# Kernel tuning notes

Hardware: AMD Instinct MI355X
Metric: run time of the kernel (lower is better)

## Reference

```python
import jax, jax.numpy as jnp
import numpy as np

B = 1_000_000   # batched RHS evaluation points
T = 1461        # days of forcing data (~4 years)
H = 16          # hidden width of ET_net / Q_net


def _step(x):
    # step_fct from models.common_net: smooth Heaviside
    return (jnp.tanh(5.0 * x) + 1.0) * 0.5


def _mlp(x, w1, b1, w2, b2, w3, b3):
    h = jnp.tanh(x @ w1 + b1)
    h = jnp.tanh(h @ w2 + b2)
    return (h @ w3 + b3)[:, 0]


def setup_inputs() -> dict:
    key = jax.random.key(0)
    ks = jax.random.split(key, 12)
    inp = {}
    inp["t"] = jax.random.uniform(ks[0], (B,), jnp.float32) * (T - 1)
    # S[:,0]=S_snow, S[:,1]=S_water  (storages in mm)
    inp["S"] = jax.random.uniform(ks[1], (B, 2), jnp.float32) * 500.0
    inp["ts"] = jnp.arange(T, dtype=jnp.float32)
    inp["precp_series"] = jax.random.uniform(ks[2], (T,), jnp.float32) * 20.0
    inp["temp_series"] = jax.random.uniform(ks[3], (T,), jnp.float32) * 30.0 - 10.0
    inp["lday_series"] = jax.random.uniform(ks[4], (T,), jnp.float32) * 0.2 + 0.3

    def lin(k, i, o):
        return jax.random.normal(k, (i, o), jnp.float32) * (1.0 / np.sqrt(i))

    inp["et_w1"] = lin(ks[5], 3, H); inp["et_b1"] = jnp.zeros((H,), jnp.float32)
    inp["et_w2"] = lin(ks[6], H, H); inp["et_b2"] = jnp.zeros((H,), jnp.float32)
    inp["et_w3"] = lin(ks[7], H, 1); inp["et_b3"] = jnp.zeros((1,), jnp.float32)
    inp["q_w1"] = lin(ks[8], 2, H); inp["q_b1"] = jnp.zeros((H,), jnp.float32)
    inp["q_w2"] = lin(ks[9], H, H); inp["q_b2"] = jnp.zeros((H,), jnp.float32)
    inp["q_w3"] = lin(ks[10], H, 1); inp["q_b3"] = jnp.zeros((1,), jnp.float32)
    # physics params: f, Smax, Qmax, Df, Tmax, Tmin
    inp["f"] = jnp.float32(0.5)
    inp["Smax"] = jnp.float32(1000.0)
    inp["Qmax"] = jnp.float32(20.0)
    inp["Df"] = jnp.float32(2.0)
    inp["Tmax"] = jnp.float32(1.0)
    inp["Tmin"] = jnp.float32(-1.0)
    return inp


def reference(t, S, ts, precp_series, temp_series, lday_series,
              et_w1, et_b1, et_w2, et_b2, et_w3, et_b3,
              q_w1, q_b1, q_w2, q_b2, q_w3, q_b3,
              f, Smax, Qmax, Df, Tmax, Tmin):
    # clamp_parameters()
    f = jnp.clip(f, 0.0, 1.0)
    Smax = jnp.clip(Smax, 100.0, 1500.0)
    Qmax = jnp.clip(Qmax, 10.0, 50.0)
    Df = jnp.clip(Df, 0.01, 5.0)
    Tmax = jnp.clip(Tmax, 0.0, 3.0)
    Tmin = jnp.clip(Tmin, -3.0, 0.0)

    # forcing interpolation (interp.evaluate(t))
    precp = jnp.interp(t, ts, precp_series)
    temp = jnp.interp(t, ts, temp_series)
    lday = jnp.interp(t, ts, lday_series)

    S_snow, S_water = S[:, 0], S[:, 1]

    ET = _mlp(jnp.stack([S_snow, S_water, temp], axis=-1),
              et_w1, et_b1, et_w2, et_b2, et_w3, et_b3)  # [B]
    Q = _mlp(jnp.stack([S_water, precp], axis=-1),
             q_w1, q_b1, q_w2, q_b2, q_w3, q_b3)          # [B]

    # M: snowmelt
    melt = _step(temp - Tmax) * _step(S_snow) * jnp.minimum(S_snow, Df * (temp - Tmax))
    # Ps / Pr: snow / rain partition of precipitation
    dS_1 = _step(Tmin - temp) * precp - melt
    dS_2 = (_step(temp - Tmin) * precp + melt
            - _step(S_water) * lday * jnp.exp(ET)
            - _step(S_water) * jnp.exp(Q))
    return jnp.stack([dS_1, dS_2], axis=-1)  # [B, 2]
```

## Files before the change

### kernel.cpp

```cpp
#include <hip/hip_runtime.h>

#define TLEN 1461
#define L2E      1.44269504088896340736f
#define TWO_L2E  2.88539008177792681472f

typedef __bf16 bf16x8 __attribute__((ext_vector_type(8)));
typedef float f32x16 __attribute__((ext_vector_type(16)));

union FragU { unsigned u[4]; bf16x8 f; };

__device__ __forceinline__ float tanh_pre(float y) {
    float e = __builtin_amdgcn_exp2f(y);
    return fmaf(-2.0f, __builtin_amdgcn_rcpf(e + 1.0f), 1.0f);
}
__device__ __forceinline__ float step_fn(float x) {
    float e = __builtin_amdgcn_exp2f(x * -14.4269504088896341f);
    return __builtin_amdgcn_rcpf(1.0f + e);
}
__device__ __forceinline__ unsigned cvt_pk_bf16(float lo, float hi) {
    unsigned r;
    asm("v_cvt_pk_bf16_f32 %0, %1, %2" : "=v"(r) : "v"(lo), "v"(hi));
    return r;
}
__device__ __forceinline__ void plswap(unsigned &a, unsigned &b) {
    asm("v_permlane32_swap_b32 %0, %1" : "+v"(a), "+v"(b));
}
__device__ __forceinline__ float plswap_add(float a, float b) {
    unsigned ua = __float_as_uint(a), ub = __float_as_uint(b);
    plswap(ua, ub);
    return __uint_as_float(ua) + __uint_as_float(ub);
}

__device__ __forceinline__ void pack_b(const float h[16], FragU &ba, FragU &bb) {
    unsigned lo0 = cvt_pk_bf16(h[0], h[1]),   lo1 = cvt_pk_bf16(h[2], h[3]);
    unsigned lo2 = cvt_pk_bf16(h[4], h[5]),   lo3 = cvt_pk_bf16(h[6], h[7]);
    unsigned hi0 = cvt_pk_bf16(h[8], h[9]),   hi1 = cvt_pk_bf16(h[10], h[11]);
    unsigned hi2 = cvt_pk_bf16(h[12], h[13]), hi3 = cvt_pk_bf16(h[14], h[15]);
    plswap(lo0, hi0); plswap(lo1, hi1); plswap(lo2, hi2); plswap(lo3, hi3);
    ba.u[0] = lo0; ba.u[1] = lo1; ba.u[2] = lo2; ba.u[3] = lo3;
    bb.u[0] = hi0; bb.u[1] = hi1; bb.u[2] = hi2; bb.u[3] = hi3;
}

__device__ __forceinline__ float tail(const FragU a2, const float jb[8],
                                      const float w3v[8], float b3half,
                                      const FragU ba, const FragU bb) {
    f32x16 c0, c1;
#pragma unroll
    for (int r = 0; r < 8; ++r) { c0[r] = jb[r]; c1[r] = jb[r]; }
    c0 = __builtin_amdgcn_mfma_f32_32x32x16_bf16(a2.f, ba.f, c0, 0, 0, 0);
    c1 = __builtin_amdgcn_mfma_f32_32x32x16_bf16(a2.f, bb.f, c1, 0, 0, 0);

    float p0 = b3half, p1 = b3half;
#pragma unroll
    for (int r = 0; r < 8; ++r) {
        p0 = fmaf(tanh_pre(c0[r]), w3v[r], p0);
        p1 = fmaf(tanh_pre(c1[r]), w3v[r], p1);
    }
    return plswap_add(p0, p1);
}

__global__ __launch_bounds__(256) void hydro_kernel(
    const float* __restrict__ g_t,
    const float* __restrict__ g_S,
    const float* __restrict__ g_precp,
    const float* __restrict__ g_temp,
    const float* __restrict__ g_lday,
    const float* __restrict__ g_ew1, const float* __restrict__ g_eb1,
    const float* __restrict__ g_ew2, const float* __restrict__ g_eb2,
    const float* __restrict__ g_ew3, const float* __restrict__ g_eb3,
    const float* __restrict__ g_qw1, const float* __restrict__ g_qb1,
    const float* __restrict__ g_qw2, const float* __restrict__ g_qb2,
    const float* __restrict__ g_qw3, const float* __restrict__ g_qb3,
    const float* __restrict__ g_Df, const float* __restrict__ g_Tmax,
    const float* __restrict__ g_Tmin,
    float* __restrict__ g_out, int B)
{
    __shared__ __align__(16) float4 s_tbl[TLEN];

    const int tx = threadIdx.x;
    for (int i = tx; i < TLEN; i += 256) {
        s_tbl[i] = make_float4(g_precp[i], g_temp[i], g_lday[i], 0.0f);
    }
    __syncthreads();

    const int lane = tx & 63;
    const int m  = lane & 31;
    const int kg = lane >> 5;

    FragU a2e, a2q;
#pragma unroll
    for (int p = 0; p < 4; ++p) {
        const int k0 = 8 * kg + 2 * p, k1 = k0 + 1;
        const int mm = (m < 16) ? m : 0;
        const float s = (m < 16) ? TWO_L2E : 0.0f;
        a2e.u[p] = cvt_pk_bf16(s * g_ew2[k0 * 16 + mm], s * g_ew2[k1 * 16 + mm]);
        a2q.u[p] = cvt_pk_bf16(s * g_qw2[k0 * 16 + mm], s * g_qw2[k1 * 16 + mm]);
    }
    float jbe[8], jbq[8], w3ve[8], w3vq[8];
#pragma unroll
    for (int r = 0; r < 8; ++r) {
        const int j = (r & 3) + 8 * (r >> 2) + 4 * kg;
        jbe[r]  = TWO_L2E * g_eb2[j];
        jbq[r]  = TWO_L2E * g_qb2[j];
        w3ve[r] = L2E * g_ew3[j];
        w3vq[r] = L2E * g_qw3[j];
    }
    const float b3e_half = (kg == 0) ? L2E * g_eb3[0] : 0.0f;
    const float b3q_half = (kg == 0) ? L2E * g_qb3[0] : 0.0f;

    const float Df   = fminf(fmaxf(g_Df[0],   0.01f), 5.0f);
    const float Tmax = fminf(fmaxf(g_Tmax[0], 0.0f),  3.0f);
    const float Tmin = fminf(fmaxf(g_Tmin[0], -3.0f), 0.0f);

    const int i = blockIdx.x * 256 + tx;
    const int ic = (i < B) ? i : (B - 1);

    const float tv = g_t[ic];
    const float2 Sv = reinterpret_cast<const float2*>(g_S)[ic];
    const float S_snow = Sv.x, S_water = Sv.y;

    int idx = (int)tv;
    idx = max(0, min(idx, TLEN - 2));
    const float fr = tv - (float)idx;
    const float4 t0 = s_tbl[idx];
    const float4 t1 = s_tbl[idx + 1];
    const float precp = fmaf(fr, t1.x - t0.x, t0.x);
    const float temp  = fmaf(fr, t1.y - t0.y, t0.y);
    const float lday  = fmaf(fr, t1.z - t0.z, t0.z);

    float h1e[16], h1q[16];
#pragma unroll
    for (int j4 = 0; j4 < 4; ++j4) {
        float4 b4 = *reinterpret_cast<const float4*>(&g_eb1[j4 * 4]);
        float4 w0 = *reinterpret_cast<const float4*>(&g_ew1[0 * 16 + j4 * 4]);
        float4 w1 = *reinterpret_cast<const float4*>(&g_ew1[1 * 16 + j4 * 4]);
        float4 w2 = *reinterpret_cast<const float4*>(&g_ew1[2 * 16 + j4 * 4]);
        h1e[j4 * 4 + 0] = tanh_pre(TWO_L2E * fmaf(temp, w2.x, fmaf(S_water, w1.x, fmaf(S_snow, w0.x, b4.x))));
        h1e[j4 * 4 + 1] = tanh_pre(TWO_L2E * fmaf(temp, w2.y, fmaf(S_water, w1.y, fmaf(S_snow, w0.y, b4.y))));
        h1e[j4 * 4 + 2] = tanh_pre(TWO_L2E * fmaf(temp, w2.z, fmaf(S_water, w1.z, fmaf(S_snow, w0.z, b4.z))));
        h1e[j4 * 4 + 3] = tanh_pre(TWO_L2E * fmaf(temp, w2.w, fmaf(S_water, w1.w, fmaf(S_snow, w0.w, b4.w))));
    }
#pragma unroll
    for (int j4 = 0; j4 < 4; ++j4) {
        float4 b4 = *reinterpret_cast<const float4*>(&g_qb1[j4 * 4]);
        float4 w0 = *reinterpret_cast<const float4*>(&g_qw1[0 * 16 + j4 * 4]);
        float4 w1 = *reinterpret_cast<const float4*>(&g_qw1[1 * 16 + j4 * 4]);
        h1q[j4 * 4 + 0] = tanh_pre(TWO_L2E * fmaf(precp, w1.x, fmaf(S_water, w0.x, b4.x)));
        h1q[j4 * 4 + 1] = tanh_pre(TWO_L2E * fmaf(precp, w1.y, fmaf(S_water, w0.y, b4.y)));
        h1q[j4 * 4 + 2] = tanh_pre(TWO_L2E * fmaf(precp, w1.z, fmaf(S_water, w0.z, b4.z)));
        h1q[j4 * 4 + 3] = tanh_pre(TWO_L2E * fmaf(precp, w1.w, fmaf(S_water, w0.w, b4.w)));
    }

    FragU bae, bbe, baq, bbq;
    pack_b(h1e, bae, bbe);
    pack_b(h1q, baq, bbq);

    const float ETs = tail(a2e, jbe, w3ve, b3e_half, bae, bbe);
    const float Qs  = tail(a2q, jbq, w3vq, b3q_half, baq, bbq);

    const float sw_step = step_fn(S_water);
    const float melt = step_fn(temp - Tmax) * step_fn(S_snow)
                     * fminf(S_snow, Df * (temp - Tmax));
    const float dS1 = step_fn(Tmin - temp) * precp - melt;
    const float dS2 = step_fn(temp - Tmin) * precp + melt
                    - sw_step * lday * __builtin_amdgcn_exp2f(ETs)
                    - sw_step * __builtin_amdgcn_exp2f(Qs);

    if (i < B) {
        reinterpret_cast<float2*>(g_out)[i] = make_float2(dS1, dS2);
    }
}

extern "C" void kernel_launch(void* const* d_in, const int* in_sizes, int n_in,
                              void* d_out, int out_size, void* d_ws, size_t ws_size,
                              hipStream_t stream)
{
    const int B = in_sizes[0];
    const int block = 256;
    const int grid = (B + block - 1) / block;
    hipLaunchKernelGGL(hydro_kernel, dim3(grid), dim3(block), 0, stream,
        (const float*)d_in[0],
        (const float*)d_in[1],
        (const float*)d_in[3],
        (const float*)d_in[4],
        (const float*)d_in[5],
        (const float*)d_in[6],  (const float*)d_in[7],
        (const float*)d_in[8],  (const float*)d_in[9],
        (const float*)d_in[10], (const float*)d_in[11],
        (const float*)d_in[12], (const float*)d_in[13],
        (const float*)d_in[14], (const float*)d_in[15],
        (const float*)d_in[16], (const float*)d_in[17],
        (const float*)d_in[21],
        (const float*)d_in[22],
        (const float*)d_in[23],
        (float*)d_out, B);
}
```

Baseline: 28.78 us.

## Process two samples per thread and fold tanh affine terms into weights

Each thread now handles two batch points, so the per-block setup (shared forcing table fill, weight fragment construction) is amortised over 512 samples and the grid is halved. The layer-3 tanh is rewritten as a sigmoid form, with its -2 scale and +1 offset folded into the output weights and bias, which removes an FMA per hidden unit. Layer-1 tanh values are packed to bf16 as soon as they are computed, and the snow/rain split reuses one step evaluation as 1-sp. Two independent sample pipelines per thread raise register pressure and may lower occupancy, and the block count falls to roughly 2k.

```diff
diff --git a/kernel.cpp b/kernel.cpp
--- a/kernel.cpp
+++ b/kernel.cpp
@@ -9,10 +9,6 @@
 
 union FragU { unsigned u[4]; bf16x8 f; };
 
-__device__ __forceinline__ float tanh_pre(float y) {
-    float e = __builtin_amdgcn_exp2f(y);
-    return fmaf(-2.0f, __builtin_amdgcn_rcpf(e + 1.0f), 1.0f);
-}
 __device__ __forceinline__ float step_fn(float x) {
     float e = __builtin_amdgcn_exp2f(x * -14.4269504088896341f);
     return __builtin_amdgcn_rcpf(1.0f + e);
@@ -31,18 +27,20 @@
     return __uint_as_float(ua) + __uint_as_float(ub);
 }
 
-__device__ __forceinline__ void pack_b(const float h[16], FragU &ba, FragU &bb) {
-    unsigned lo0 = cvt_pk_bf16(h[0], h[1]),   lo1 = cvt_pk_bf16(h[2], h[3]);
-    unsigned lo2 = cvt_pk_bf16(h[4], h[5]),   lo3 = cvt_pk_bf16(h[6], h[7]);
-    unsigned hi0 = cvt_pk_bf16(h[8], h[9]),   hi1 = cvt_pk_bf16(h[10], h[11]);
-    unsigned hi2 = cvt_pk_bf16(h[12], h[13]), hi3 = cvt_pk_bf16(h[14], h[15]);
-    plswap(lo0, hi0); plswap(lo1, hi1); plswap(lo2, hi2); plswap(lo3, hi3);
-    ba.u[0] = lo0; ba.u[1] = lo1; ba.u[2] = lo2; ba.u[3] = lo3;
-    bb.u[0] = hi0; bb.u[1] = hi1; bb.u[2] = hi2; bb.u[3] = hi3;
+__device__ __forceinline__ void quad_tanh_pack(float y0, float y1, float y2, float y3,
+                                               unsigned &wlo, unsigned &whi) {
+    float s0 = __builtin_amdgcn_rcpf(1.0f + __builtin_amdgcn_exp2f(y0));
+    float s1 = __builtin_amdgcn_rcpf(1.0f + __builtin_amdgcn_exp2f(y1));
+    float s2 = __builtin_amdgcn_rcpf(1.0f + __builtin_amdgcn_exp2f(y2));
+    float s3 = __builtin_amdgcn_rcpf(1.0f + __builtin_amdgcn_exp2f(y3));
+    float h0 = fmaf(-2.0f, s0, 1.0f), h1 = fmaf(-2.0f, s1, 1.0f);
+    float h2 = fmaf(-2.0f, s2, 1.0f), h3 = fmaf(-2.0f, s3, 1.0f);
+    wlo = cvt_pk_bf16(h0, h1);
+    whi = cvt_pk_bf16(h2, h3);
 }
 
 __device__ __forceinline__ float tail(const FragU a2, const float jb[8],
-                                      const float w3v[8], float b3half,
+                                      const float w3n[8], float pinit,
                                       const FragU ba, const FragU bb) {
     f32x16 c0, c1;
 #pragma unroll
@@ -50,13 +48,93 @@
     c0 = __builtin_amdgcn_mfma_f32_32x32x16_bf16(a2.f, ba.f, c0, 0, 0, 0);
     c1 = __builtin_amdgcn_mfma_f32_32x32x16_bf16(a2.f, bb.f, c1, 0, 0, 0);
 
-    float p0 = b3half, p1 = b3half;
+    float p0 = pinit, p1 = pinit;
 #pragma unroll
     for (int r = 0; r < 8; ++r) {
-        p0 = fmaf(tanh_pre(c0[r]), w3v[r], p0);
-        p1 = fmaf(tanh_pre(c1[r]), w3v[r], p1);
+        float s0 = __builtin_amdgcn_rcpf(1.0f + __builtin_amdgcn_exp2f(c0[r]));
+        float s1 = __builtin_amdgcn_rcpf(1.0f + __builtin_amdgcn_exp2f(c1[r]));
+        p0 = fmaf(w3n[r], s0, p0);
+        p1 = fmaf(w3n[r], s1, p1);
     }
     return plswap_add(p0, p1);
+}
+
+struct Weights {
+    FragU a2e, a2q;
+    float jbe[8], jbq[8], w3ne[8], w3nq[8];
+    float pinit_e, pinit_q;
+    float Df, Tmax, Tmin;
+};
+
+__device__ __forceinline__ float2 sample_pipeline(
+    float tv, float S_snow, float S_water,
+    const float4* __restrict__ s_tbl, const Weights &W,
+    const float* __restrict__ g_ew1, const float* __restrict__ g_eb1,
+    const float* __restrict__ g_qw1, const float* __restrict__ g_qb1)
+{
+    int idx = (int)tv;
+    idx = max(0, min(idx, TLEN - 2));
+    const float fr = tv - (float)idx;
+    const float4 t0 = s_tbl[idx];
+    const float4 t1 = s_tbl[idx + 1];
+    const float precp = fmaf(fr, t1.x - t0.x, t0.x);
+    const float temp  = fmaf(fr, t1.y - t0.y, t0.y);
+    const float lday  = fmaf(fr, t1.z - t0.z, t0.z);
+
+    unsigned elo[4], ehi[4], qlo[4], qhi[4];
+#pragma unroll
+    for (int j4 = 0; j4 < 4; ++j4) {
+        float4 b4 = *reinterpret_cast<const float4*>(&g_eb1[j4 * 4]);
+        float4 w0 = *reinterpret_cast<const float4*>(&g_ew1[0 * 16 + j4 * 4]);
+        float4 w1 = *reinterpret_cast<const float4*>(&g_ew1[1 * 16 + j4 * 4]);
+        float4 w2 = *reinterpret_cast<const float4*>(&g_ew1[2 * 16 + j4 * 4]);
+        float y0 = TWO_L2E * fmaf(temp, w2.x, fmaf(S_water, w1.x, fmaf(S_snow, w0.x, b4.x)));
+        float y1 = TWO_L2E * fmaf(temp, w2.y, fmaf(S_water, w1.y, fmaf(S_snow, w0.y, b4.y)));
+        float y2 = TWO_L2E * fmaf(temp, w2.z, fmaf(S_water, w1.z, fmaf(S_snow, w0.z, b4.z)));
+        float y3 = TWO_L2E * fmaf(temp, w2.w, fmaf(S_water, w1.w, fmaf(S_snow, w0.w, b4.w)));
+        unsigned wl, wh;
+        quad_tanh_pack(y0, y1, y2, y3, wl, wh);
+        if (j4 < 2) { elo[j4 * 2] = wl; elo[j4 * 2 + 1] = wh; }
+        else        { ehi[(j4 - 2) * 2] = wl; ehi[(j4 - 2) * 2 + 1] = wh; }
+    }
+#pragma unroll
+    for (int j4 = 0; j4 < 4; ++j4) {
+        float4 b4 = *reinterpret_cast<const float4*>(&g_qb1[j4 * 4]);
+        float4 w0 = *reinterpret_cast<const float4*>(&g_qw1[0 * 16 + j4 * 4]);
+        float4 w1 = *reinterpret_cast<const float4*>(&g_qw1[1 * 16 + j4 * 4]);
+        float y0 = TWO_L2E * fmaf(precp, w1.x, fmaf(S_water, w0.x, b4.x));
+        float y1 = TWO_L2E * fmaf(precp, w1.y, fmaf(S_water, w0.y, b4.y));
+        float y2 = TWO_L2E * fmaf(precp, w1.z, fmaf(S_water, w0.z, b4.z));
+        float y3 = TWO_L2E * fmaf(precp, w1.w, fmaf(S_water, w0.w, b4.w));
+        unsigned wl, wh;
+        quad_tanh_pack(y0, y1, y2, y3, wl, wh);
+        if (j4 < 2) { qlo[j4 * 2] = wl; qlo[j4 * 2 + 1] = wh; }
+        else        { qhi[(j4 - 2) * 2] = wl; qhi[(j4 - 2) * 2 + 1] = wh; }
+    }
+
+    FragU bae, bbe, baq, bbq;
+#pragma unroll
+    for (int p = 0; p < 4; ++p) {
+        unsigned l = elo[p], h = ehi[p];
+        plswap(l, h);
+        bae.u[p] = l; bbe.u[p] = h;
+        l = qlo[p]; h = qhi[p];
+        plswap(l, h);
+        baq.u[p] = l; bbq.u[p] = h;
+    }
+
+    const float ETs = tail(W.a2e, W.jbe, W.w3ne, W.pinit_e, bae, bbe);
+    const float Qs  = tail(W.a2q, W.jbq, W.w3nq, W.pinit_q, baq, bbq);
+
+    const float sw_step = step_fn(S_water);
+    const float sp      = step_fn(temp - W.Tmin);
+    const float melt = step_fn(temp - W.Tmax) * step_fn(S_snow)
+                     * fminf(S_snow, W.Df * (temp - W.Tmax));
+    const float dS1 = (1.0f - sp) * precp - melt;
+    const float dS2 = sp * precp + melt
+                    - sw_step * fmaf(lday, __builtin_amdgcn_exp2f(ETs),
+                                     __builtin_amdgcn_exp2f(Qs));
+    return make_float2(dS1, dS2);
 }
 
 __global__ __launch_bounds__(256) void hydro_kernel(
@@ -87,88 +165,50 @@
     const int m  = lane & 31;
     const int kg = lane >> 5;
 
-    FragU a2e, a2q;
+    Weights W;
 #pragma unroll
     for (int p = 0; p < 4; ++p) {
         const int k0 = 8 * kg + 2 * p, k1 = k0 + 1;
         const int mm = (m < 16) ? m : 0;
         const float s = (m < 16) ? TWO_L2E : 0.0f;
-        a2e.u[p] = cvt_pk_bf16(s * g_ew2[k0 * 16 + mm], s * g_ew2[k1 * 16 + mm]);
-        a2q.u[p] = cvt_pk_bf16(s * g_qw2[k0 * 16 + mm], s * g_qw2[k1 * 16 + mm]);
-    }
-    float jbe[8], jbq[8], w3ve[8], w3vq[8];
+        W.a2e.u[p] = cvt_pk_bf16(s * g_ew2[k0 * 16 + mm], s * g_ew2[k1 * 16 + mm]);
+        W.a2q.u[p] = cvt_pk_bf16(s * g_qw2[k0 * 16 + mm], s * g_qw2[k1 * 16 + mm]);
+    }
+    float sum_e = 0.0f, sum_q = 0.0f;
 #pragma unroll
     for (int r = 0; r < 8; ++r) {
         const int j = (r & 3) + 8 * (r >> 2) + 4 * kg;
-        jbe[r]  = TWO_L2E * g_eb2[j];
-        jbq[r]  = TWO_L2E * g_qb2[j];
-        w3ve[r] = L2E * g_ew3[j];
-        w3vq[r] = L2E * g_qw3[j];
-    }
-    const float b3e_half = (kg == 0) ? L2E * g_eb3[0] : 0.0f;
-    const float b3q_half = (kg == 0) ? L2E * g_qb3[0] : 0.0f;
-
-    const float Df   = fminf(fmaxf(g_Df[0],   0.01f), 5.0f);
-    const float Tmax = fminf(fmaxf(g_Tmax[0], 0.0f),  3.0f);
-    const float Tmin = fminf(fmaxf(g_Tmin[0], -3.0f), 0.0f);
-
-    const int i = blockIdx.x * 256 + tx;
-    const int ic = (i < B) ? i : (B - 1);
-
-    const float tv = g_t[ic];
-    const float2 Sv = reinterpret_cast<const float2*>(g_S)[ic];
-    const float S_snow = Sv.x, S_water = Sv.y;
-
-    int idx = (int)tv;
-    idx = max(0, min(idx, TLEN - 2));
-    const float fr = tv - (float)idx;
-    const float4 t0 = s_tbl[idx];
-    const float4 t1 = s_tbl[idx + 1];
-    const float precp = fmaf(fr, t1.x - t0.x, t0.x);
-    const float temp  = fmaf(fr, t1.y - t0.y, t0.y);
-    const float lday  = fmaf(fr, t1.z - t0.z, t0.z);
-
-    float h1e[16], h1q[16];
-#pragma unroll
-    for (int j4 = 0; j4 < 4; ++j4) {
-        float4 b4 = *reinterpret_cast<const float4*>(&g_eb1[j4 * 4]);
-        float4 w0 = *reinterpret_cast<const float4*>(&g_ew1[0 * 16 + j4 * 4]);
-        float4 w1 = *reinterpret_cast<const float4*>(&g_ew1[1 * 16 + j4 * 4]);
-        float4 w2 = *reinterpret_cast<const float4*>(&g_ew1[2 * 16 + j4 * 4]);
-        h1e[j4 * 4 + 0] = tanh_pre(TWO_L2E * fmaf(temp, w2.x, fmaf(S_water, w1.x, fmaf(S_snow, w0.x, b4.x))));
-        h1e[j4 * 4 + 1] = tanh_pre(TWO_L2E * fmaf(temp, w2.y, fmaf(S_water, w1.y, fmaf(S_snow, w0.y, b4.y))));
-        h1e[j4 * 4 + 2] = tanh_pre(TWO_L2E * fmaf(temp, w2.z, fmaf(S_water, w1.z, fmaf(S_snow, w0.z, b4.z))));
-        h1e[j4 * 4 + 3] = tanh_pre(TWO_L2E * fmaf(temp, w2.w, fmaf(S_water, w1.w, fmaf(S_snow, w0.w, b4.w))));
-    }
-#pragma unroll
-    for (int j4 = 0; j4 < 4; ++j4) {
-        float4 b4 = *reinterpret_cast<const float4*>(&g_qb1[j4 * 4]);
-        float4 w0 = *reinterpret_cast<const float4*>(&g_qw1[0 * 16 + j4 * 4]);
-        float4 w1 = *reinterpret_cast<const float4*>(&g_qw1[1 * 16 + j4 * 4]);
-        h1q[j4 * 4 + 0] = tanh_pre(TWO_L2E * fmaf(precp, w1.x, fmaf(S_water, w0.x, b4.x)));
-        h1q[j4 * 4 + 1] = tanh_pre(TWO_L2E * fmaf(precp, w1.y, fmaf(S_water, w0.y, b4.y)));
-        h1q[j4 * 4 + 2] = tanh_pre(TWO_L2E * fmaf(precp, w1.z, fmaf(S_water, w0.z, b4.z)));
-        h1q[j4 * 4 + 3] = tanh_pre(TWO_L2E * fmaf(precp, w1.w, fmaf(S_water, w0.w, b4.w)));
-    }
-
-    FragU bae, bbe, baq, bbq;
-    pack_b(h1e, bae, bbe);
-    pack_b(h1q, baq, bbq);
-
-    const float ETs = tail(a2e, jbe, w3ve, b3e_half, bae, bbe);
-    const float Qs  = tail(a2q, jbq, w3vq, b3q_half, baq, bbq);
-
-    const float sw_step = step_fn(S_water);
-    const float melt = step_fn(temp - Tmax) * step_fn(S_snow)
-                     * fminf(S_snow, Df * (temp - Tmax));
-    const float dS1 = step_fn(Tmin - temp) * precp - melt;
-    const float dS2 = step_fn(temp - Tmin) * precp + melt
-                    - sw_step * lday * __builtin_amdgcn_exp2f(ETs)
-                    - sw_step * __builtin_amdgcn_exp2f(Qs);
-
-    if (i < B) {
-        reinterpret_cast<float2*>(g_out)[i] = make_float2(dS1, dS2);
-    }
+        W.jbe[r] = TWO_L2E * g_eb2[j];
+        W.jbq[r] = TWO_L2E * g_qb2[j];
+        const float w3e = g_ew3[j], w3q = g_qw3[j];
+        sum_e += w3e; sum_q += w3q;
+        W.w3ne[r] = -2.0f * L2E * w3e;
+        W.w3nq[r] = -2.0f * L2E * w3q;
+    }
+    W.pinit_e = L2E * fmaf(0.5f, g_eb3[0], sum_e);
+    W.pinit_q = L2E * fmaf(0.5f, g_qb3[0], sum_q);
+
+    W.Df   = fminf(fmaxf(g_Df[0],   0.01f), 5.0f);
+    W.Tmax = fminf(fmaxf(g_Tmax[0], 0.0f),  3.0f);
+    W.Tmin = fminf(fmaxf(g_Tmin[0], -3.0f), 0.0f);
+
+    const int i0 = blockIdx.x * 512 + tx;
+    const int i1 = i0 + 256;
+    const int c0i = (i0 < B) ? i0 : (B - 1);
+    const int c1i = (i1 < B) ? i1 : (B - 1);
+
+    const float tv0 = g_t[c0i];
+    const float tv1 = g_t[c1i];
+    const float2 Sv0 = reinterpret_cast<const float2*>(g_S)[c0i];
+    const float2 Sv1 = reinterpret_cast<const float2*>(g_S)[c1i];
+
+    const float2 r0 = sample_pipeline(tv0, Sv0.x, Sv0.y, s_tbl, W,
+                                      g_ew1, g_eb1, g_qw1, g_qb1);
+    const float2 r1 = sample_pipeline(tv1, Sv1.x, Sv1.y, s_tbl, W,
+                                      g_ew1, g_eb1, g_qw1, g_qb1);
+
+    if (i0 < B) reinterpret_cast<float2*>(g_out)[i0] = r0;
+    if (i1 < B) reinterpret_cast<float2*>(g_out)[i1] = r1;
 }
 
 extern "C" void kernel_launch(void* const* d_in, const int* in_sizes, int n_in,
@@ -177,7 +217,7 @@
 {
     const int B = in_sizes[0];
     const int block = 256;
-    const int grid = (B + block - 1) / block;
+    const int grid = (B + 511) / 512;
     hipLaunchKernelGGL(hydro_kernel, dim3(grid), dim3(block), 0, stream,
         (const float*)d_in[0],
         (const float*)d_in[1],
```

New measurement: 26.69 us. 7.3% less time.
